# Optimization experiments

Hardware: AMD Instinct MI355X
Metric: run time of the kernel (lower is better)

The kernel has to match this reference:

```python
import jax, jax.numpy as jnp
import numpy as np

B, S, D, H, FF = 4, 1024, 1024, 8, 4096
DK = D // H
EPS = 1e-5


def layernorm(x, g, b):
    m = jnp.mean(x, axis=-1, keepdims=True)
    v = jnp.mean(jnp.square(x - m), axis=-1, keepdims=True)
    return (x - m) * jax.lax.rsqrt(v + EPS) * g + b


def setup_inputs() -> dict:
    key = jax.random.key(0)
    ks = jax.random.split(key, 8)
    w = lambda k, shape: jax.random.normal(k, shape, jnp.float32) * 0.02
    return {
        "x": jax.random.normal(ks[0], (B, S, D), jnp.float32),
        "mask": jnp.ones((B, 1, 1, S), jnp.int32),  # unused in 'infer' mode, kept for fidelity
        "g1": jnp.ones((D,), jnp.float32), "b1": jnp.zeros((D,), jnp.float32),
        "Wq": w(ks[1], (D, D)), "bq": jnp.zeros((D,), jnp.float32),
        "Wk": w(ks[2], (D, D)), "bk": jnp.zeros((D,), jnp.float32),
        "Wv": w(ks[3], (D, H * D)), "bv": jnp.zeros((H * D,), jnp.float32),
        "g2": jnp.ones((D,), jnp.float32), "b2": jnp.zeros((D,), jnp.float32),
        "W1": w(ks[4], (D, FF)), "bw1": jnp.zeros((FF,), jnp.float32),
        "W2": w(ks[5], (FF, D)), "bw2": jnp.zeros((D,), jnp.float32),
    }


def reference(x, mask, g1, b1, Wq, bq, Wk, bk, Wv, bv, g2, b2, W1, bw1, W2, bw2):
    # --- MultiHeadedAttention (mode='infer'; mask is ignored by this path) ---
    xn = layernorm(x, g1, b1)                                   # [B,S,D]
    q = (xn @ Wq + bq).reshape(B, S, H, DK).transpose(0, 2, 1, 3)  # [B,H,S,DK]
    k = (xn @ Wk + bk).reshape(B, S, H, DK).transpose(0, 2, 1, 3)  # [B,H,S,DK]
    v = (xn @ Wv + bv).reshape(B, S, H, D).transpose(0, 2, 1, 3)   # [B,H,S,D]
    scores = jnp.einsum('bhqd,bhkd->bhqk', q, k) / jnp.sqrt(jnp.float32(DK))
    p = jax.nn.softmax(scores, axis=-1)                          # [B,H,S,S]
    ctx = jnp.einsum('bhqk,bhkd->bhqd', p, v)                    # [B,H,S,D]
    # Source does x.view(-1, B, dim, h).sum(heads).view(B, S, dim) on the
    # contiguous [B,H,S,D] tensor: a raw row-major reshape, reproduced exactly.
    attn_out = ctx.reshape(S, B, D, H).sum(axis=-1).reshape(B, S, D)
    # --- residual + SublayerConnection (pre-norm GELU FFN) ---
    x1 = x + attn_out
    xn2 = layernorm(x1, g2, b2)
    ffn = jax.nn.gelu(xn2 @ W1 + bw1, approximate=False) @ W2 + bw2
    return x1 + ffn
```

## Files before the change

### kernel.cpp

```cpp
#include <hip/hip_runtime.h>
#include <hip/hip_bf16.h>
#include <math.h>

typedef __attribute__((ext_vector_type(8))) short   short8;
typedef __attribute__((ext_vector_type(4))) short   short4v;
typedef __attribute__((ext_vector_type(8))) __bf16  bf16x8;
typedef __attribute__((ext_vector_type(4))) float   f32x4;

typedef const __attribute__((address_space(1))) void cgv_t;
typedef __attribute__((address_space(3))) void lv_t;

__device__ __forceinline__ float bs2f(short s) {
  unsigned int u = ((unsigned int)(unsigned short)s) << 16;
  return __builtin_bit_cast(float, u);
}
__device__ __forceinline__ short f2bs(float f) {
  __hip_bfloat16 h = __float2bfloat16(f);
  return __builtin_bit_cast(short, h);
}
__device__ __forceinline__ void glds16(const short* g, short* l) {
  __builtin_amdgcn_global_load_lds((cgv_t*)g, (lv_t*)l, 16, 0, 0);
}


__global__ __launch_bounds__(256) void transpose_k(const float* __restrict__ in,
                                                   short* __restrict__ out,
                                                   int R, int C) {
  __shared__ __align__(16) short T[64 * 72];
  const int r0 = blockIdx.y * 64, c0 = blockIdx.x * 64;
  const int t = threadIdx.x;
  {
    const int rr = t >> 4;
    const int cc = (t & 15) << 2;
#pragma unroll
    for (int h = 0; h < 4; h++) {
      const int row = rr + h * 16;
      f32x4 v = *(const f32x4*)(in + (long)(r0 + row) * C + c0 + cc);
#pragma unroll
      for (int e = 0; e < 4; e++) T[row * 72 + cc + e] = f2bs(v[e]);
    }
  }
  __syncthreads();
  {
    const int cr = t >> 3;
    const int rs = (t & 7) << 3;
#pragma unroll
    for (int h = 0; h < 2; h++) {
      const int c = cr + h * 32;
      short8 v;
#pragma unroll
      for (int e = 0; e < 8; e++) v[e] = T[(rs + e) * 72 + c];
      *(short8*)(out + (long)(c0 + c) * R + r0 + rs) = v;
    }
  }
}

__global__ __launch_bounds__(256) void wv8_k(const float* __restrict__ Wv,
                                             short* __restrict__ out) {
  __shared__ __align__(16) short T[64 * 72];
  const int r0 = blockIdx.x * 64, k0 = blockIdx.y * 64;
  const int t = threadIdx.x;
  const int wave = t >> 6, lane = t & 63;
  const int r = r0 + lane;
#pragma unroll 4
  for (int i = 0; i < 16; i++) {
    const int k = k0 + wave * 16 + i;
    const float* src = Wv + (long)k * 8192 + 8 * r;
    f32x4 a = *(const f32x4*)src;
    f32x4 b = *(const f32x4*)(src + 4);
    float s = (a[0] + a[1] + a[2] + a[3]) + (b[0] + b[1] + b[2] + b[3]);
    T[lane * 72 + wave * 16 + i] = f2bs(s);
  }
  __syncthreads();
  const int rr = t >> 3, kc = (t & 7) << 3;
#pragma unroll
  for (int half = 0; half < 2; half++) {
    const int rl = rr + half * 32;
    *(short8*)(out + (long)(r0 + rl) * 1024 + k0 + kc) = *(const short8*)&T[rl * 72 + kc];
  }
}

__global__ __launch_bounds__(256) void bv8_k(const float* __restrict__ bv,
                                             float* __restrict__ out) {
  const int r = blockIdx.x * 256 + threadIdx.x;
  f32x4 a = *(const f32x4*)(bv + 8 * r);
  f32x4 b = *(const f32x4*)(bv + 8 * r + 4);
  out[r] = (a[0] + a[1] + a[2] + a[3]) + (b[0] + b[1] + b[2] + b[3]);
}

__global__ __launch_bounds__(256) void ln_k(const float* __restrict__ in,
                                            const float* __restrict__ g,
                                            const float* __restrict__ b,
                                            short* __restrict__ out) {
  const int t = threadIdx.x;
  const long base = (long)blockIdx.x * 1024 + t * 4;
  f32x4 f = *(const f32x4*)(in + base);
  float v[4] = {f[0], f[1], f[2], f[3]};
  float s1 = v[0] + v[1] + v[2] + v[3];
  float s2 = v[0]*v[0] + v[1]*v[1] + v[2]*v[2] + v[3]*v[3];
#pragma unroll
  for (int off = 32; off; off >>= 1) {
    s1 += __shfl_xor(s1, off);
    s2 += __shfl_xor(s2, off);
  }
  __shared__ float rs[4], rq[4];
  if ((t & 63) == 0) { rs[t >> 6] = s1; rq[t >> 6] = s2; }
  __syncthreads();
  s1 = rs[0] + rs[1] + rs[2] + rs[3];
  s2 = rq[0] + rq[1] + rq[2] + rq[3];
  const float mean = s1 * (1.0f / 1024.0f);
  const float var  = s2 * (1.0f / 1024.0f) - mean * mean;
  const float rstd = rsqrtf(var + 1e-5f);
  f32x4 gv = *(const f32x4*)(g + t * 4);
  f32x4 bv = *(const f32x4*)(b + t * 4);
  short4v o;
#pragma unroll
  for (int i = 0; i < 4; i++)
    o[i] = f2bs((v[i] - mean) * rstd * gv[i] + bv[i]);
  *(short4v*)(out + base) = o;
}

__global__ __launch_bounds__(256) void reduce2_k(const float* __restrict__ p0,
                                                 const float* __restrict__ p1,
                                                 const float* __restrict__ x1,
                                                 const float* __restrict__ bias,
                                                 float* __restrict__ out) {
  const int t = threadIdx.x;
  const long base = (long)blockIdx.x * 1024 + t * 4;
  f32x4 a = *(const f32x4*)(p0 + base);
  f32x4 b = *(const f32x4*)(p1 + base);
  f32x4 c = *(const f32x4*)(x1 + base);
  f32x4 d = *(const f32x4*)(bias + t * 4);
  *(f32x4*)(out + base) = a + b + c + d;
}

__global__ __launch_bounds__(256, 2) void flash_k(
    const short* __restrict__ Qg_, const short* __restrict__ Kg_,
    const short* __restrict__ V8T, const float* __restrict__ xg,
    float* __restrict__ x1) {
  __shared__ __align__(16) short smem[40960];
  short* Qs = smem;
  short* Ks = smem + 8192;
  short* Vs = smem + 24576;

  const int t = threadIdx.x;
  const int wave = t >> 6, lane = t & 63;
  const int llo = lane & 15, lhi = lane >> 4;
  const int q0 = blockIdx.x * 64;
  const int bh = blockIdx.y, b = bh >> 3, h = bh & 7;
  const float SC = 0.0883883476483184f;

  const short* Qg = Qg_ + ((long)(b * 1024 + q0)) * 1024 + h * 128;
  const short* Kg = Kg_ + ((long)b * 1024) * 1024 + h * 128;
  const short* Vg = V8T + (long)bh * 131072;

  const int srow = t >> 2, schunk = (t & 3) << 3;
  const int wbase = wave * 512;
  const int arow = (wave * 16 + llo) * 32 + lhi * 8;

#pragma unroll
  for (int kk = 0; kk < 4; kk++)
    glds16(Qg + (long)srow * 1024 + kk * 32 + schunk, Qs + kk * 2048 + wbase);

  f32x4 o[8];
  float mR[4], lR[4];
#pragma unroll
  for (int i = 0; i < 8; i++) o[i] = f32x4{0.f, 0.f, 0.f, 0.f};
#pragma unroll
  for (int r = 0; r < 4; r++) { mR[r] = -1e30f; lR[r] = 0.f; }

  for (int it = 0; it < 8; it++) {
    const int kt0 = it * 128;
#pragma unroll
    for (int kk = 0; kk < 4; kk++) {
      glds16(Kg + (long)(kt0 + srow) * 1024 + kk * 32 + schunk,
             Ks + kk * 4096 + wbase);
      glds16(Kg + (long)(kt0 + 64 + srow) * 1024 + kk * 32 + schunk,
             Ks + kk * 4096 + 2048 + wbase);
      glds16(Vg + (long)srow * 1024 + kt0 + kk * 32 + schunk,
             Vs + kk * 4096 + wbase);
      glds16(Vg + (long)(64 + srow) * 1024 + kt0 + kk * 32 + schunk,
             Vs + kk * 4096 + 2048 + wbase);
    }
    __syncthreads();

    f32x4 s[8];
#pragma unroll
    for (int i = 0; i < 8; i++) s[i] = f32x4{0.f, 0.f, 0.f, 0.f};
#pragma unroll
    for (int kk = 0; kk < 4; kk++) {
      bf16x8 aq = *(const bf16x8*)(Qs + kk * 2048 + arow);
#pragma unroll
      for (int ct = 0; ct < 8; ct++) {
        bf16x8 bk = *(const bf16x8*)(Ks + kk * 4096 + (ct * 16 + llo) * 32 + lhi * 8);
        s[ct] = __builtin_amdgcn_mfma_f32_16x16x32_bf16(aq, bk, s[ct], 0, 0, 0);
      }
    }
#pragma unroll
    for (int ct = 0; ct < 8; ct++)
#pragma unroll
      for (int r = 0; r < 4; r++) s[ct][r] *= SC;
    float alpha[4];
#pragma unroll
    for (int r = 0; r < 4; r++) {
      float mt = s[0][r];
#pragma unroll
      for (int ct = 1; ct < 8; ct++) mt = fmaxf(mt, s[ct][r]);
      mt = fmaxf(mt, __shfl_xor(mt, 1));
      mt = fmaxf(mt, __shfl_xor(mt, 2));
      mt = fmaxf(mt, __shfl_xor(mt, 4));
      mt = fmaxf(mt, __shfl_xor(mt, 8));
      const float mn = fmaxf(mR[r], mt);
      alpha[r] = expf(mR[r] - mn);
      mR[r] = mn;
    }
#pragma unroll
    for (int ct = 0; ct < 8; ct++)
#pragma unroll
      for (int r = 0; r < 4; r++) s[ct][r] = expf(s[ct][r] - mR[r]);
#pragma unroll
    for (int ct = 0; ct < 8; ct++)
#pragma unroll
      for (int r = 0; r < 4; r++) o[ct][r] *= alpha[r];
#pragma unroll
    for (int r = 0; r < 4; r++) {
      float ls = s[0][r];
#pragma unroll
      for (int ct = 1; ct < 8; ct++) ls += s[ct][r];
      ls += __shfl_xor(ls, 1);
      ls += __shfl_xor(ls, 2);
      ls += __shfl_xor(ls, 4);
      ls += __shfl_xor(ls, 8);
      lR[r] = lR[r] * alpha[r] + ls;
    }
    __syncthreads();

#pragma unroll
    for (int ct = 0; ct < 8; ct++) {
      const int base = (ct >> 1) * 4096 + ((ct & 1) << 4) + llo;
#pragma unroll
      for (int r = 0; r < 4; r++)
        Ks[base + (wave * 16 + lhi * 4 + r) * 32] = f2bs(s[ct][r]);
    }
    __syncthreads();

#pragma unroll
    for (int kk = 0; kk < 4; kk++) {
      bf16x8 ap = *(const bf16x8*)(Ks + kk * 4096 + arow);
#pragma unroll
      for (int ct = 0; ct < 8; ct++) {
        bf16x8 bv = *(const bf16x8*)(Vs + kk * 4096 + (ct * 16 + llo) * 32 + lhi * 8);
        o[ct] = __builtin_amdgcn_mfma_f32_16x16x32_bf16(ap, bv, o[ct], 0, 0, 0);
      }
    }
    __syncthreads();
  }

  float inv[4];
#pragma unroll
  for (int r = 0; r < 4; r++) inv[r] = 1.0f / lR[r];
#pragma unroll
  for (int ct = 0; ct < 8; ct++) {
#pragma unroll
    for (int r = 0; r < 4; r++) {
      const int row = q0 + wave * 16 + lhi * 4 + r;
      const long idx = ((long)(b * 8 + h) * 1024 + row) * 128 + ct * 16 + llo;
      x1[idx] = xg[idx] + o[ct][r] * inv[r];
    }
  }
}

enum { EPI_GELU = 4, EPI_QKV8 = 6, EPI_PART = 8 };

template <int EPI, int BN, int NS>
__global__ __launch_bounds__(256) void gemm128(
    const short* __restrict__ A, int lda, long azh, long azl,
    const short* __restrict__ Bt, int ldb, long bzh, long bzl,
    const float* __restrict__ bias, long biasl,
    void* __restrict__ outp, long czl, int ldc,
    const void* __restrict__ aux,
    int K) {
  constexpr int WH = (BN == 128) ? 64 : 32;
  constexpr int RT = WH / 16;
  constexpr int ASLAB = 4096;
  constexpr int BSLAB = BN * 32;
  constexpr int STAGE = NS * (ASLAB + BSLAB);
  constexpr int SMEM_SHORTS = (EPI == EPI_QKV8 && STAGE < 17408) ? 17408 : STAGE;
  __shared__ __align__(16) short smem[SMEM_SHORTS];
  short* As = smem;
  short* Bs = smem + NS * ASLAB;

  const int t = threadIdx.x;
  const int wave = t >> 6, lane = t & 63;
  const int llo = lane & 15, lhi = lane >> 4;
  const int wm = (BN == 128) ? (wave >> 1) : wave;
  const int wn = (BN == 128) ? (wave & 1) : 0;
  const int bn0 = blockIdx.x * BN, bm0 = blockIdx.y * 128;
  const int z = blockIdx.z;
  const int zh = z >> 3, zl = z & 7;

  const short* Ab = A + (long)zh * azh + (long)zl * azl;
  const short* Bb = Bt + (long)zh * bzh + (long)zl * bzl;
  bias += (long)zl * biasl;

  f32x4 acc[RT][4];
#pragma unroll
  for (int i = 0; i < RT; i++)
#pragma unroll
    for (int j = 0; j < 4; j++) acc[i][j] = f32x4{0.f, 0.f, 0.f, 0.f};

  const int srow = t >> 2, schunk = (t & 3) << 3;
  const short* Ag0 = Ab + (long)(bm0 + srow) * lda + schunk;
  const short* Ag1 = Ab + (long)(bm0 + 64 + srow) * lda + schunk;
  const short* Bg0 = Bb + (long)(bn0 + srow) * ldb + schunk;
  const short* Bg1 = Bb + (long)(bn0 + 64 + srow) * ldb + schunk;
  short* AsW0 = As + (wave * 16) * 32;
  short* AsW1 = As + (64 + wave * 16) * 32;
  short* BsW0 = Bs + (wave * 16) * 32;
  short* BsW1 = Bs + (64 + wave * 16) * 32;

  const short* aRd = As + (wm * WH + llo) * 32 + lhi * 8;
  const short* bRd = Bs + (wn * 64 + llo) * 32 + lhi * 8;

  for (int kt = 0; kt < K; kt += 32 * NS) {
#pragma unroll
    for (int s = 0; s < NS; s++) {
      glds16(Ag0 + kt + s * 32, AsW0 + s * ASLAB);
      glds16(Ag1 + kt + s * 32, AsW1 + s * ASLAB);
      glds16(Bg0 + kt + s * 32, BsW0 + s * BSLAB);
      if (BN == 128) glds16(Bg1 + kt + s * 32, BsW1 + s * BSLAB);
    }
    __syncthreads();
#pragma unroll
    for (int s = 0; s < NS; s++) {
      bf16x8 af[RT], bf[4];
#pragma unroll
      for (int i = 0; i < RT; i++)
        af[i] = *(const bf16x8*)(aRd + s * ASLAB + i * 16 * 32);
#pragma unroll
      for (int j = 0; j < 4; j++)
        bf[j] = *(const bf16x8*)(bRd + s * BSLAB + j * 16 * 32);
#pragma unroll
      for (int rt = 0; rt < RT; rt++)
#pragma unroll
        for (int ct = 0; ct < 4; ct++)
          acc[rt][ct] = __builtin_amdgcn_mfma_f32_16x16x32_bf16(af[rt], bf[ct], acc[rt][ct], 0, 0, 0);
    }
    __syncthreads();
  }

  if (EPI == EPI_GELU || (EPI == EPI_QKV8 && blockIdx.z < 2)) {
    short* C = (short*)outp + (long)z * czl;
#pragma unroll
    for (int ct = 0; ct < 4; ct++) {
      const int col = bn0 + wn * 64 + ct * 16 + llo;
      const float bval = bias[col];
#pragma unroll
      for (int rt = 0; rt < RT; rt++) {
#pragma unroll
        for (int r = 0; r < 4; r++) {
          const int row = bm0 + wm * WH + rt * 16 + lhi * 4 + r;
          float v = acc[rt][ct][r] + bval;
          if (EPI == EPI_GELU) v = 0.5f * v * (1.0f + erff(v * 0.70710678118654752f));
          C[(long)row * ldc + col] = f2bs(v);
        }
      }
    }
  } else if (EPI == EPI_QKV8) {
    short* Ts = smem;
#pragma unroll
    for (int ct = 0; ct < 4; ct++) {
      const int c = wn * 64 + ct * 16 + llo;
      const float bval = bias[bn0 + c];
#pragma unroll
      for (int rt = 0; rt < RT; rt++) {
#pragma unroll
        for (int r = 0; r < 4; r++) {
          const int row = wm * WH + rt * 16 + lhi * 4 + r;
          Ts[c * 136 + row] = f2bs(acc[rt][ct][r] + bval);
        }
      }
    }
    __syncthreads();
    const int bb = bm0 >> 10, s0 = bm0 & 1023, head = bn0 >> 7;
    short* dstbase = (short*)aux + ((long)(bb * 8 + head)) * 131072 + s0;
    const int sc8 = (t & 15) << 3;
    const int cb = t >> 4;
#pragma unroll
    for (int j = 0; j < 8; j++) {
      const int c = cb + j * 16;
      *(short8*)(dstbase + (long)c * 1024 + sc8) = *(const short8*)&Ts[c * 136 + sc8];
    }
  } else if (EPI == EPI_PART) {
    float* C = (float*)outp + (long)z * czl;
#pragma unroll
    for (int ct = 0; ct < 4; ct++) {
      const int col = bn0 + wn * 64 + ct * 16 + llo;
#pragma unroll
      for (int rt = 0; rt < RT; rt++) {
#pragma unroll
        for (int r = 0; r < 4; r++) {
          const int row = bm0 + wm * WH + rt * 16 + lhi * 4 + r;
          C[(long)row * ldc + col] = acc[rt][ct][r];
        }
      }
    }
  }
}

#define MF16(va, vb, vc) __builtin_amdgcn_mfma_f32_16x16x32_bf16(va, vb, vc, 0, 0, 0)
#define FENCE asm volatile("" ::: "memory")
#define BARRIER do { FENCE; __builtin_amdgcn_s_barrier(); FENCE; } while (0)
#define VMW(n) asm volatile("s_waitcnt vmcnt(" #n ")" ::: "memory")
#define NOPS ((void)0)

#define STAGE_A(BUF, KH, KB) do {                                          \
    glds16(Ag + (KB), smem + ((BUF) * 2 + (KH)) * 8192 + wofs);            \
    glds16(Ag2 + (KB), smem + ((BUF) * 2 + (KH)) * 8192 + 4096 + wofs);    \
  } while (0)
#define STAGE_B(BUF, KH, KB) do {                                          \
    glds16(Bg + (KB), smem + 32768 + ((BUF) * 2 + (KH)) * 8192 + wofs);    \
    glds16(Bg2 + (KB), smem + 32768 + ((BUF) * 2 + (KH)) * 8192 + 4096 + wofs); \
  } while (0)

#define PHASE(RH, KH, BUF, STAGE_STMT, WAIT_STMT)                          \
  {                                                                        \
    const short* Ar_ = smem + ((BUF) * 2 + (KH)) * 8192 + aoff + (RH) * 2048; \
    const short* Br_ = smem + 32768 + ((BUF) * 2 + (KH)) * 8192 + boff;    \
    bf16x8 a0 = *(const bf16x8*)(Ar_);                                     \
    bf16x8 a1 = *(const bf16x8*)(Ar_ + 512);                               \
    bf16x8 a2 = *(const bf16x8*)(Ar_ + 1024);                              \
    bf16x8 a3 = *(const bf16x8*)(Ar_ + 1536);                              \
    bf16x8 b0 = *(const bf16x8*)(Br_);                                     \
    bf16x8 b1 = *(const bf16x8*)(Br_ + 512);                               \
    bf16x8 b2 = *(const bf16x8*)(Br_ + 1024);                              \
    bf16x8 b3 = *(const bf16x8*)(Br_ + 1536);                              \
    STAGE_STMT;                                                            \
    BARRIER;                                                               \
    __builtin_amdgcn_s_setprio(1);                                         \
    acc[(RH) * 4 + 0][0] = MF16(a0, b0, acc[(RH) * 4 + 0][0]);             \
    acc[(RH) * 4 + 0][1] = MF16(a0, b1, acc[(RH) * 4 + 0][1]);             \
    acc[(RH) * 4 + 0][2] = MF16(a0, b2, acc[(RH) * 4 + 0][2]);             \
    acc[(RH) * 4 + 0][3] = MF16(a0, b3, acc[(RH) * 4 + 0][3]);             \
    acc[(RH) * 4 + 1][0] = MF16(a1, b0, acc[(RH) * 4 + 1][0]);             \
    acc[(RH) * 4 + 1][1] = MF16(a1, b1, acc[(RH) * 4 + 1][1]);             \
    acc[(RH) * 4 + 1][2] = MF16(a1, b2, acc[(RH) * 4 + 1][2]);             \
    acc[(RH) * 4 + 1][3] = MF16(a1, b3, acc[(RH) * 4 + 1][3]);             \
    acc[(RH) * 4 + 2][0] = MF16(a2, b0, acc[(RH) * 4 + 2][0]);             \
    acc[(RH) * 4 + 2][1] = MF16(a2, b1, acc[(RH) * 4 + 2][1]);             \
    acc[(RH) * 4 + 2][2] = MF16(a2, b2, acc[(RH) * 4 + 2][2]);             \
    acc[(RH) * 4 + 2][3] = MF16(a2, b3, acc[(RH) * 4 + 2][3]);             \
    acc[(RH) * 4 + 3][0] = MF16(a3, b0, acc[(RH) * 4 + 3][0]);             \
    acc[(RH) * 4 + 3][1] = MF16(a3, b1, acc[(RH) * 4 + 3][1]);             \
    acc[(RH) * 4 + 3][2] = MF16(a3, b2, acc[(RH) * 4 + 3][2]);             \
    acc[(RH) * 4 + 3][3] = MF16(a3, b3, acc[(RH) * 4 + 3][3]);             \
    __builtin_amdgcn_s_setprio(0);                                         \
    WAIT_STMT;                                                             \
    BARRIER;                                                               \
  }

#define TILE8(T, BUF)                                                      \
  PHASE(0, 0, BUF, STAGE_A(1 - (BUF), 1, ((T) + 1) * 64 + 32), NOPS);      \
  PHASE(1, 0, BUF, STAGE_B(1 - (BUF), 1, ((T) + 1) * 64 + 32), VMW(8));    \
  PHASE(0, 1, BUF, STAGE_A(BUF, 0, ((T) + 2) * 64), NOPS);                 \
  PHASE(1, 1, BUF, STAGE_B(BUF, 0, ((T) + 2) * 64), VMW(8))

__global__ __launch_bounds__(512, 2) void gemm256_gelu(
    const short* __restrict__ A, int lda,
    const short* __restrict__ Bt, int ldb,
    const float* __restrict__ bias,
    short* __restrict__ C, int ldc, int K) {
  __shared__ __align__(16) short smem[65536];

  const int t = threadIdx.x;
  const int wave = t >> 6, lane = t & 63;
  const int llo = lane & 15, lhi = lane >> 4;
  const int wm = wave >> 2, wn = wave & 3;
  const int bm0 = blockIdx.y * 256, bn0 = blockIdx.x * 256;

  const int srow = t >> 2;
  const int sgc = (((t & 3) ^ ((t >> 3) & 3)) << 3);
  const short* Ag  = A  + (long)(bm0 + srow) * lda + sgc;
  const short* Ag2 = A  + (long)(bm0 + 128 + srow) * lda + sgc;
  const short* Bg  = Bt + (long)(bn0 + srow) * ldb + sgc;
  const short* Bg2 = Bt + (long)(bn0 + 128 + srow) * ldb + sgc;
  const int wofs = wave * 512;

  const int swz = ((lhi ^ ((llo >> 1) & 3)) << 3);
  const int aoff = (wm * 128 + llo) * 32 + swz;
  const int boff = (wn * 64 + llo) * 32 + swz;

  f32x4 acc[8][4];
#pragma unroll
  for (int i = 0; i < 8; i++)
#pragma unroll
    for (int j = 0; j < 4; j++) acc[i][j] = f32x4{0.f, 0.f, 0.f, 0.f};

  const int NT = K >> 6;

  STAGE_A(0, 0, 0);  STAGE_B(0, 0, 0);
  STAGE_A(0, 1, 32); STAGE_B(0, 1, 32);
  STAGE_A(1, 0, 64); STAGE_B(1, 0, 64);
  VMW(8);
  BARRIER;

  for (int tt = 0; tt < NT - 2; tt += 2) {
    TILE8(tt, 0);
    TILE8(tt + 1, 1);
  }
  PHASE(0, 0, 0, STAGE_A(1, 1, (NT - 1) * 64 + 32), NOPS);
  PHASE(1, 0, 0, STAGE_B(1, 1, (NT - 1) * 64 + 32), VMW(8));
  PHASE(0, 1, 0, NOPS, NOPS);
  PHASE(1, 1, 0, NOPS, VMW(4));
  PHASE(0, 0, 1, NOPS, NOPS);
  PHASE(1, 0, 1, NOPS, VMW(0));
  PHASE(0, 1, 1, NOPS, NOPS);
  PHASE(1, 1, 1, NOPS, NOPS);

#pragma unroll
  for (int ct = 0; ct < 4; ct++) {
    const int col = bn0 + wn * 64 + ct * 16 + llo;
    const float bval = bias[col];
#pragma unroll
    for (int rt = 0; rt < 8; rt++) {
#pragma unroll
      for (int r = 0; r < 4; r++) {
        const int row = bm0 + wm * 128 + rt * 16 + lhi * 4 + r;
        float v = acc[rt][ct][r] + bval;
        v = 0.5f * v * (1.0f + erff(v * 0.70710678118654752f));
        C[(long)row * ldc + col] = f2bs(v);
      }
    }
  }
}

extern "C" void kernel_launch(void* const* d_in, const int* in_sizes, int n_in,
                              void* d_out, int out_size, void* d_ws, size_t ws_size,
                              hipStream_t stream) {
  const float* x   = (const float*)d_in[0];
  const float* g1  = (const float*)d_in[2];
  const float* b1  = (const float*)d_in[3];
  const float* Wq  = (const float*)d_in[4];
  const float* bq  = (const float*)d_in[5];
  const float* Wk  = (const float*)d_in[6];
  const float* bk  = (const float*)d_in[7];
  const float* Wv  = (const float*)d_in[8];
  const float* bv  = (const float*)d_in[9];
  const float* g2  = (const float*)d_in[10];
  const float* b2  = (const float*)d_in[11];
  const float* W1  = (const float*)d_in[12];
  const float* bw1 = (const float*)d_in[13];
  const float* W2  = (const float*)d_in[14];
  const float* bw2 = (const float*)d_in[15];

  char* ws = (char*)d_ws;
  const long MB = 1024 * 1024;
  float* bQKV = (float*)(ws);
  float* x1   = (float*)(ws + 1 * MB);
  short* wqT  = (short*)(ws + 17 * MB);
  short* wkT  = (short*)(ws + 19 * MB);
  short* wv8T = (short*)(ws + 21 * MB);
  short* xn   = (short*)(ws + 23 * MB);
  short* Q    = (short*)(ws + 31 * MB);
  short* Kb   = (short*)(ws + 39 * MB);
  short* V8T  = (short*)(ws + 47 * MB);
  short* xn2  = (short*)(ws + 17 * MB);
  short* Hb   = (short*)(ws + 25 * MB);
  short* w1T  = (short*)(ws + 57 * MB);
  short* w2T  = (short*)(ws + 65 * MB);
  float* part = (float*)(ws + 73 * MB);

  hipMemcpyAsync(bQKV, bq, 4096, hipMemcpyDeviceToDevice, stream);
  hipMemcpyAsync(bQKV + 1024, bk, 4096, hipMemcpyDeviceToDevice, stream);
  bv8_k<<<4, 256, 0, stream>>>(bv, bQKV + 2048);

  transpose_k<<<dim3(16, 16), 256, 0, stream>>>(Wq, wqT, 1024, 1024);
  transpose_k<<<dim3(16, 16), 256, 0, stream>>>(Wk, wkT, 1024, 1024);
  wv8_k<<<dim3(16, 16), 256, 0, stream>>>(Wv, wv8T);

  ln_k<<<4096, 256, 0, stream>>>(x, g1, b1, xn);

  gemm128<EPI_QKV8, 128, 2><<<dim3(8, 32, 3), 256, 0, stream>>>(
      xn, 1024, 0, 0, wqT, 1024, 0, 1048576, bQKV, 1024,
      Q, 4194304, 1024, V8T, 1024);

  flash_k<<<dim3(16, 32), 256, 0, stream>>>(Q, Kb, V8T, x, x1);

  transpose_k<<<dim3(64, 16), 256, 0, stream>>>(W1, w1T, 1024, 4096);
  transpose_k<<<dim3(16, 64), 256, 0, stream>>>(W2, w2T, 4096, 1024);

  ln_k<<<4096, 256, 0, stream>>>(x1, g2, b2, xn2);

  gemm256_gelu<<<dim3(16, 16), 512, 0, stream>>>(
      xn2, 1024, w1T, 1024, bw1, Hb, 4096, 1024);

  gemm128<EPI_PART, 64, 2><<<dim3(16, 32, 2), 256, 0, stream>>>(
      Hb, 4096, 0, 2048, w2T, 4096, 0, 2048, nullptr, 0,
      part, 4194304, 1024, nullptr, 2048);

  reduce2_k<<<4096, 256, 0, stream>>>(part, part + 4194304, x1, bw2,
                                      (float*)d_out);
}
```

Baseline: 406.5 us.

## Reuse B fragments across row halves and stage GELU epilogue through LDS

In the 256x256 GELU GEMM main loop, the B-operand fragments are loaded from LDS only in the first row-half phase and reused in the second, which halves the B LDS reads. The compiler memory fences around barriers are replaced with sched_barrier plus an explicit lgkmcnt wait, to control instruction scheduling. The epilogue now writes bias+GELU bf16 results into a padded per-wave LDS slab and then stores rows with 16-byte coalesced global writes instead of scattered 2-byte stores. This adds register pressure for the persistent B fragments and relies on the hand-placed waits for correctness.

After: 398.6 us. No clear change (-2.0%).

```diff
diff --git a/kernel.cpp b/kernel.cpp
--- a/kernel.cpp
+++ b/kernel.cpp
@@ -409,8 +409,6 @@
 }
 
 #define MF16(va, vb, vc) __builtin_amdgcn_mfma_f32_16x16x32_bf16(va, vb, vc, 0, 0, 0)
-#define FENCE asm volatile("" ::: "memory")
-#define BARRIER do { FENCE; __builtin_amdgcn_s_barrier(); FENCE; } while (0)
 #define VMW(n) asm volatile("s_waitcnt vmcnt(" #n ")" ::: "memory")
 #define NOPS ((void)0)
 
@@ -423,47 +421,53 @@
     glds16(Bg2 + (KB), smem + 32768 + ((BUF) * 2 + (KH)) * 8192 + 4096 + wofs); \
   } while (0)
 
-#define PHASE(RH, KH, BUF, STAGE_STMT, WAIT_STMT)                          \
+#define PHASE(RH, KH, BUF, LOADB, STAGE_STMT, WAIT_STMT)                   \
   {                                                                        \
     const short* Ar_ = smem + ((BUF) * 2 + (KH)) * 8192 + aoff + (RH) * 2048; \
-    const short* Br_ = smem + 32768 + ((BUF) * 2 + (KH)) * 8192 + boff;    \
     bf16x8 a0 = *(const bf16x8*)(Ar_);                                     \
     bf16x8 a1 = *(const bf16x8*)(Ar_ + 512);                               \
     bf16x8 a2 = *(const bf16x8*)(Ar_ + 1024);                              \
     bf16x8 a3 = *(const bf16x8*)(Ar_ + 1536);                              \
-    bf16x8 b0 = *(const bf16x8*)(Br_);                                     \
-    bf16x8 b1 = *(const bf16x8*)(Br_ + 512);                               \
-    bf16x8 b2 = *(const bf16x8*)(Br_ + 1024);                              \
-    bf16x8 b3 = *(const bf16x8*)(Br_ + 1536);                              \
+    if (LOADB) {                                                           \
+      const short* Br_ = smem + 32768 + ((BUF) * 2 + (KH)) * 8192 + boff;  \
+      vb0 = *(const bf16x8*)(Br_);                                         \
+      vb1 = *(const bf16x8*)(Br_ + 512);                                   \
+      vb2 = *(const bf16x8*)(Br_ + 1024);                                  \
+      vb3 = *(const bf16x8*)(Br_ + 1536);                                  \
+    }                                                                      \
     STAGE_STMT;                                                            \
-    BARRIER;                                                               \
+    __builtin_amdgcn_sched_barrier(0);                                     \
+    __builtin_amdgcn_s_barrier();                                          \
+    asm volatile("s_waitcnt lgkmcnt(0)" ::: "memory");                     \
+    __builtin_amdgcn_sched_barrier(0);                                     \
     __builtin_amdgcn_s_setprio(1);                                         \
-    acc[(RH) * 4 + 0][0] = MF16(a0, b0, acc[(RH) * 4 + 0][0]);             \
-    acc[(RH) * 4 + 0][1] = MF16(a0, b1, acc[(RH) * 4 + 0][1]);             \
-    acc[(RH) * 4 + 0][2] = MF16(a0, b2, acc[(RH) * 4 + 0][2]);             \
-    acc[(RH) * 4 + 0][3] = MF16(a0, b3, acc[(RH) * 4 + 0][3]);             \
-    acc[(RH) * 4 + 1][0] = MF16(a1, b0, acc[(RH) * 4 + 1][0]);             \
-    acc[(RH) * 4 + 1][1] = MF16(a1, b1, acc[(RH) * 4 + 1][1]);             \
-    acc[(RH) * 4 + 1][2] = MF16(a1, b2, acc[(RH) * 4 + 1][2]);             \
-    acc[(RH) * 4 + 1][3] = MF16(a1, b3, acc[(RH) * 4 + 1][3]);             \
-    acc[(RH) * 4 + 2][0] = MF16(a2, b0, acc[(RH) * 4 + 2][0]);             \
-    acc[(RH) * 4 + 2][1] = MF16(a2, b1, acc[(RH) * 4 + 2][1]);             \
-    acc[(RH) * 4 + 2][2] = MF16(a2, b2, acc[(RH) * 4 + 2][2]);             \
-    acc[(RH) * 4 + 2][3] = MF16(a2, b3, acc[(RH) * 4 + 2][3]);             \
-    acc[(RH) * 4 + 3][0] = MF16(a3, b0, acc[(RH) * 4 + 3][0]);             \
-    acc[(RH) * 4 + 3][1] = MF16(a3, b1, acc[(RH) * 4 + 3][1]);             \
-    acc[(RH) * 4 + 3][2] = MF16(a3, b2, acc[(RH) * 4 + 3][2]);             \
-    acc[(RH) * 4 + 3][3] = MF16(a3, b3, acc[(RH) * 4 + 3][3]);             \
+    acc[(RH) * 4 + 0][0] = MF16(a0, vb0, acc[(RH) * 4 + 0][0]);            \
+    acc[(RH) * 4 + 0][1] = MF16(a0, vb1, acc[(RH) * 4 + 0][1]);            \
+    acc[(RH) * 4 + 0][2] = MF16(a0, vb2, acc[(RH) * 4 + 0][2]);            \
+    acc[(RH) * 4 + 0][3] = MF16(a0, vb3, acc[(RH) * 4 + 0][3]);            \
+    acc[(RH) * 4 + 1][0] = MF16(a1, vb0, acc[(RH) * 4 + 1][0]);            \
+    acc[(RH) * 4 + 1][1] = MF16(a1, vb1, acc[(RH) * 4 + 1][1]);            \
+    acc[(RH) * 4 + 1][2] = MF16(a1, vb2, acc[(RH) * 4 + 1][2]);            \
+    acc[(RH) * 4 + 1][3] = MF16(a1, vb3, acc[(RH) * 4 + 1][3]);            \
+    acc[(RH) * 4 + 2][0] = MF16(a2, vb0, acc[(RH) * 4 + 2][0]);            \
+    acc[(RH) * 4 + 2][1] = MF16(a2, vb1, acc[(RH) * 4 + 2][1]);            \
+    acc[(RH) * 4 + 2][2] = MF16(a2, vb2, acc[(RH) * 4 + 2][2]);            \
+    acc[(RH) * 4 + 2][3] = MF16(a2, vb3, acc[(RH) * 4 + 2][3]);            \
+    acc[(RH) * 4 + 3][0] = MF16(a3, vb0, acc[(RH) * 4 + 3][0]);            \
+    acc[(RH) * 4 + 3][1] = MF16(a3, vb1, acc[(RH) * 4 + 3][1]);            \
+    acc[(RH) * 4 + 3][2] = MF16(a3, vb2, acc[(RH) * 4 + 3][2]);            \
+    acc[(RH) * 4 + 3][3] = MF16(a3, vb3, acc[(RH) * 4 + 3][3]);            \
     __builtin_amdgcn_s_setprio(0);                                         \
     WAIT_STMT;                                                             \
-    BARRIER;                                                               \
-  }
-
-#define TILE8(T, BUF)                                                      \
-  PHASE(0, 0, BUF, STAGE_A(1 - (BUF), 1, ((T) + 1) * 64 + 32), NOPS);      \
-  PHASE(1, 0, BUF, STAGE_B(1 - (BUF), 1, ((T) + 1) * 64 + 32), VMW(8));    \
-  PHASE(0, 1, BUF, STAGE_A(BUF, 0, ((T) + 2) * 64), NOPS);                 \
-  PHASE(1, 1, BUF, STAGE_B(BUF, 0, ((T) + 2) * 64), VMW(8))
+    __builtin_amdgcn_sched_barrier(0);                                     \
+    __builtin_amdgcn_s_barrier();                                          \
+  }
+
+#define TILE8(T, BUF)                                                        \
+  PHASE(0, 0, BUF, 1, STAGE_A(1 - (BUF), 1, ((T) + 1) * 64 + 32), NOPS);     \
+  PHASE(1, 0, BUF, 0, STAGE_B(1 - (BUF), 1, ((T) + 1) * 64 + 32), VMW(8));   \
+  PHASE(0, 1, BUF, 1, STAGE_A(BUF, 0, ((T) + 2) * 64), NOPS);                \
+  PHASE(1, 1, BUF, 0, STAGE_B(BUF, 0, ((T) + 2) * 64), VMW(8))
 
 __global__ __launch_bounds__(512, 2) void gemm256_gelu(
     const short* __restrict__ A, int lda,
@@ -495,6 +499,7 @@
   for (int i = 0; i < 8; i++)
 #pragma unroll
     for (int j = 0; j < 4; j++) acc[i][j] = f32x4{0.f, 0.f, 0.f, 0.f};
+  bf16x8 vb0, vb1, vb2, vb3;
 
   const int NT = K >> 6;
 
@@ -502,34 +507,46 @@
   STAGE_A(0, 1, 32); STAGE_B(0, 1, 32);
   STAGE_A(1, 0, 64); STAGE_B(1, 0, 64);
   VMW(8);
-  BARRIER;
+  __builtin_amdgcn_s_barrier();
 
   for (int tt = 0; tt < NT - 2; tt += 2) {
     TILE8(tt, 0);
     TILE8(tt + 1, 1);
   }
-  PHASE(0, 0, 0, STAGE_A(1, 1, (NT - 1) * 64 + 32), NOPS);
-  PHASE(1, 0, 0, STAGE_B(1, 1, (NT - 1) * 64 + 32), VMW(8));
-  PHASE(0, 1, 0, NOPS, NOPS);
-  PHASE(1, 1, 0, NOPS, VMW(4));
-  PHASE(0, 0, 1, NOPS, NOPS);
-  PHASE(1, 0, 1, NOPS, VMW(0));
-  PHASE(0, 1, 1, NOPS, NOPS);
-  PHASE(1, 1, 1, NOPS, NOPS);
-
-#pragma unroll
-  for (int ct = 0; ct < 4; ct++) {
-    const int col = bn0 + wn * 64 + ct * 16 + llo;
-    const float bval = bias[col];
-#pragma unroll
-    for (int rt = 0; rt < 8; rt++) {
-#pragma unroll
-      for (int r = 0; r < 4; r++) {
-        const int row = bm0 + wm * 128 + rt * 16 + lhi * 4 + r;
-        float v = acc[rt][ct][r] + bval;
-        v = 0.5f * v * (1.0f + erff(v * 0.70710678118654752f));
-        C[(long)row * ldc + col] = f2bs(v);
+  PHASE(0, 0, 0, 1, STAGE_A(1, 1, (NT - 1) * 64 + 32), NOPS);
+  PHASE(1, 0, 0, 0, STAGE_B(1, 1, (NT - 1) * 64 + 32), VMW(8));
+  PHASE(0, 1, 0, 1, NOPS, NOPS);
+  PHASE(1, 1, 0, 0, NOPS, VMW(4));
+  PHASE(0, 0, 1, 1, NOPS, NOPS);
+  PHASE(1, 0, 1, 0, NOPS, VMW(0));
+  PHASE(0, 1, 1, 1, NOPS, NOPS);
+  PHASE(1, 1, 1, 0, NOPS, NOPS);
+
+  short* slab = smem + wave * 4864;
+  float bv4[4];
+#pragma unroll
+  for (int ct = 0; ct < 4; ct++) bv4[ct] = bias[bn0 + wn * 64 + ct * 16 + llo];
+  const int rl0 = lane >> 3, cb8 = (lane & 7) << 3;
+  const short* srd = slab + rl0 * 76 + cb8;
+  short* Cw = C + (long)(bm0 + wm * 128 + rl0) * ldc + bn0 + wn * 64 + cb8;
+#pragma unroll
+  for (int p = 0; p < 2; p++) {
+#pragma unroll
+    for (int rt4 = 0; rt4 < 4; rt4++) {
+#pragma unroll
+      for (int ct = 0; ct < 4; ct++) {
+#pragma unroll
+        for (int r = 0; r < 4; r++) {
+          float v = acc[p * 4 + rt4][ct][r] + bv4[ct];
+          v = 0.5f * v * (1.0f + erff(v * 0.70710678118654752f));
+          slab[(rt4 * 16 + lhi * 4 + r) * 76 + ct * 16 + llo] = f2bs(v);
+        }
       }
+    }
+#pragma unroll
+    for (int j = 0; j < 8; j++) {
+      short8 v = *(const short8*)(srd + j * 8 * 76);
+      *(short8*)(Cw + ((long)p * 64 + j * 8) * ldc) = v;
     }
   }
 }
```
